# Optimization experiments

Hardware: AMD Instinct MI355X
Metric: run time of the kernel (lower is better)

Reference implementation:

```python
import jax, jax.numpy as jnp
import numpy as np

H = 19  # input_size == hidden_size

def setup_inputs() -> dict:
    key = jax.random.key(0)
    ks = jax.random.split(key, 7)
    seq_len, batch = 2048, 1024
    s = 1.0 / np.sqrt(H)  # PyTorch default uniform(-1/sqrt(H), 1/sqrt(H))
    x = jax.random.normal(ks[0], (seq_len, batch, H), dtype=jnp.float32)
    W_ih = jax.random.uniform(ks[1], (3 * H, H), jnp.float32, -s, s)
    W_hh = jax.random.uniform(ks[2], (3 * H, H), jnp.float32, -s, s)
    b_ih = jax.random.uniform(ks[3], (3 * H,), jnp.float32, -s, s)
    b_hh = jax.random.uniform(ks[4], (3 * H,), jnp.float32, -s, s)
    W_out = jax.random.uniform(ks[5], (1, H), jnp.float32, -s, s)
    b_out = jax.random.uniform(ks[6], (1,), jnp.float32, -s, s)
    return {"x": x, "W_ih": W_ih, "W_hh": W_hh, "b_ih": b_ih,
            "b_hh": b_hh, "W_out": W_out, "b_out": b_out}

def _gru(x, W_ih, W_hh, b_ih, b_hh):
    # Precompute all input projections in one big GEMM: [T, B, 3H]
    xg = jnp.einsum('tbi,gi->tbg', x, W_ih) + b_ih
    Whr, Whz, Whn = W_hh[:H], W_hh[H:2*H], W_hh[2*H:]
    bhr, bhz, bhn = b_hh[:H], b_hh[H:2*H], b_hh[2*H:]
    h0 = jnp.zeros(x.shape[1:2] + (H,), dtype=x.dtype)

    def step(h, xg_t):
        xr, xz, xn = xg_t[:, :H], xg_t[:, H:2*H], xg_t[:, 2*H:]
        r = jax.nn.sigmoid(xr + h @ Whr.T + bhr)
        z = jax.nn.sigmoid(xz + h @ Whz.T + bhz)
        n = jnp.tanh(xn + r * (h @ Whn.T + bhn))
        h_new = (1.0 - z) * n + z * h
        return h_new, h_new

    _, r_out = jax.lax.scan(step, h0, xg)  # r_out: [T, B, H]
    return r_out

def reference(x, W_ih, W_hh, b_ih, b_hh, W_out, b_out):
    r_out = _gru(x, W_ih, W_hh, b_ih, b_hh)
    return r_out @ W_out.T + b_out  # [T, B, 1]
```

## Files before the change

kernel.cpp:

```cpp
#include <hip/hip_runtime.h>
#include <math.h>

#define HH 19
#define NB 1024
#define TT 2048

typedef float v2f __attribute__((ext_vector_type(2)));
typedef unsigned u2 __attribute__((ext_vector_type(2)));

__device__ __forceinline__ float rl(float v, int l) {
  return __uint_as_float(__builtin_amdgcn_readlane(__float_as_uint(v), l));
}
__device__ __forceinline__ float frcp(float v) {
  return __builtin_amdgcn_rcpf(v);
}
__device__ __forceinline__ float fexp2(float v) {
#if __has_builtin(__builtin_amdgcn_exp2f)
  return __builtin_amdgcn_exp2f(v);
#else
  return exp2f(v);
#endif
}
__device__ __forceinline__ v2f vfma(v2f a, v2f b, v2f c) {
#if __has_builtin(__builtin_elementwise_fma)
  return __builtin_elementwise_fma(a, b, c);
#else
  v2f r; r.x = fmaf(a.x, b.x, c.x); r.y = fmaf(a.y, b.y, c.y); return r;
#endif
}

#if __has_builtin(__builtin_amdgcn_permlane32_swap)
#define HAVE_PLS 1
__device__ __forceinline__ u2 pls(float x) {
  unsigned u = __float_as_uint(x);
  return __builtin_amdgcn_permlane32_swap(u, u, false, false);
}
#else
#define HAVE_PLS 0
#endif

__global__ void __launch_bounds__(64)
__attribute__((amdgpu_waves_per_eu(1, 1)))
gru57_v2(const float* __restrict__ x, const float* __restrict__ Wih,
         const float* __restrict__ Whh, const float* __restrict__ bih,
         const float* __restrict__ bhh, const float* __restrict__ Wout,
         const float* __restrict__ bout, float* __restrict__ out)
{
  const int b = blockIdx.x;
  const int lane = threadIdx.x;

  const float L2E = 1.4426950408889634f;

  int row;
  if (lane < 32)      row = lane;
  else if (lane < 51) row = lane + 6;
  else if (lane < 57) row = lane - 19;
  else                row = 37;
  const bool isn = (row >= 2 * HH);
  const float scale = isn ? (2.0f * L2E) : L2E;

  v2f wx2[10], wh2[10], wo2[10];
#pragma unroll
  for (int j = 0; j < 10; ++j) {
    const int k0 = 2 * j, k1 = 2 * j + 1;
    wx2[j].x = Wih[row * HH + k0] * scale;
    wx2[j].y = (k1 < HH) ? Wih[row * HH + k1] * scale : 0.0f;
    wh2[j].x = Whh[row * HH + k0] * scale;
    wh2[j].y = (k1 < HH) ? Whh[row * HH + k1] * scale : 0.0f;
    wo2[j].x = Wout[k0];
    wo2[j].y = (k1 < HH) ? Wout[k1] : 0.0f;
  }
  const float bxv = bih[row] * scale, bhv = bhh[row] * scale;
  const float ax0 = isn ? bxv : (bxv + bhv);
  const float ah0 = isn ? bhv : 0.0f;
  const float bo  = bout[0];

  const int il = lane < HH ? lane : HH - 1;
  const int zaddr = ((il < 13) ? (19 + il) : (38 + il)) * 4;

#if HAVE_PLS
  bool loIsX;
  {
    unsigned l = (unsigned)lane;
    u2 pr = __builtin_amdgcn_permlane32_swap(l, l, false, false);
    loIsX = ((unsigned)__builtin_amdgcn_readlane((int)pr.x, 32) < 32u);
  }
#else
  const int loaddr = (lane & 31) * 4;
  const int hiaddr = ((lane & 31) | 32) * 4;
#endif

  float h = 0.0f;
  v2f sh2[10];
#pragma unroll
  for (int j = 0; j < 10; ++j) { sh2[j].x = 0.0f; sh2[j].y = 0.0f; }

  int vz;
  asm("v_mov_b32 %0, 0" : "=v"(vz));

  v2f xA[10], xB[10], xC[10], xD[10];
  xA[9].y = 0.0f; xB[9].y = 0.0f; xC[9].y = 0.0f; xD[9].y = 0.0f;

#define LOADROW(dst, trow) do {                                         \
    const float* _p = x + ((size_t)(trow) * NB + b) * HH + vz;          \
    _Pragma("unroll")                                                   \
    for (int _j = 0; _j < 9; ++_j) {                                    \
      dst[_j].x = _p[2 * _j];                                           \
      dst[_j].y = _p[2 * _j + 1];                                       \
    }                                                                   \
    dst[9].x = _p[18];                                                  \
  } while (0)

  LOADROW(xA, 0); LOADROW(xB, 1); LOADROW(xC, 2); LOADROW(xD, 3);

#if HAVE_PLS
#define LOBCAST(val, dst) do { u2 _s = pls(val);                        \
    dst = __uint_as_float(loIsX ? _s.x : _s.y); } while (0)
#define HIBCAST(val, dst) do { u2 _s = pls(val);                        \
    dst = __uint_as_float(loIsX ? _s.y : _s.x); } while (0)
#else
#define LOBCAST(val, dst) dst = __uint_as_float((unsigned)               \
    __builtin_amdgcn_ds_bpermute(loaddr, (int)__float_as_uint(val)))
#define HIBCAST(val, dst) dst = __uint_as_float((unsigned)               \
    __builtin_amdgcn_ds_bpermute(hiaddr, (int)__float_as_uint(val)))
#endif

#define STEP(xv, tcur) do {                                             \
    v2f axA = {ax0, 0.0f}, axB = {0.0f, 0.0f};                          \
    v2f ahA = {ah0, 0.0f}, ahB = {0.0f, 0.0f};                          \
    _Pragma("unroll")                                                   \
    for (int _j = 0; _j < 5; ++_j) {                                    \
      axA = vfma(xv[_j], wx2[_j], axA);                                 \
      ahA = vfma(sh2[_j], wh2[_j], ahA);                                \
    }                                                                   \
    _Pragma("unroll")                                                   \
    for (int _j = 5; _j < 10; ++_j) {                                   \
      axB = vfma(xv[_j], wx2[_j], axB);                                 \
      ahB = vfma(sh2[_j], wh2[_j], ahB);                                \
    }                                                                   \
    const v2f axv = axA + axB;                                          \
    const v2f ahv = ahA + ahB;                                          \
    const float prex = axv.x + axv.y;                                   \
    const float preh = ahv.x + ahv.y;                                   \
    const float pre  = prex + preh;                                     \
    const float sig  = frcp(1.0f + fexp2(-pre));                        \
                    \
    const int zzi = __builtin_amdgcn_ds_bpermute(                       \
        zaddr, (int)__float_as_uint(sig));                              \
                                  \
    float rr; LOBCAST(sig, rr);                                         \
    const float npre = fmaf(rr, preh, prex);                            \
    const float nn = fmaf(-2.0f, frcp(fexp2(npre) + 1.0f), 1.0f);       \
                                  \
    float nh; HIBCAST(nn, nh);                                          \
    const float zz = __uint_as_float((unsigned)zzi);                    \
    h = fmaf(zz, h - nh, nh);                                           \
    _Pragma("unroll")                                                   \
    for (int _j = 0; _j < 9; ++_j) {                                    \
      sh2[_j].x = rl(h, 2 * _j);                                        \
      sh2[_j].y = rl(h, 2 * _j + 1);                                    \
    }                                                                   \
    sh2[9].x = rl(h, 18); sh2[9].y = 0.0f;                              \
    v2f oA = {bo, 0.0f}, oB = {0.0f, 0.0f};                             \
    _Pragma("unroll")                                                   \
    for (int _j = 0; _j < 5; ++_j) oA = vfma(sh2[_j], wo2[_j], oA);     \
    _Pragma("unroll")                                                   \
    for (int _j = 5; _j < 10; ++_j) oB = vfma(sh2[_j], wo2[_j], oB);    \
    const v2f ov = oA + oB;                                             \
    if (lane == 0) out[(size_t)(tcur) * NB + b] = ov.x + ov.y;          \
  } while (0)

  for (int t = 0; t < TT; t += 4) {
    STEP(xA, t);
    { const int tn = (t + 4 < TT) ? t + 4 : TT - 1; LOADROW(xA, tn); }
    STEP(xB, t + 1);
    { const int tn = (t + 5 < TT) ? t + 5 : TT - 1; LOADROW(xB, tn); }
    STEP(xC, t + 2);
    { const int tn = (t + 6 < TT) ? t + 6 : TT - 1; LOADROW(xC, tn); }
    STEP(xD, t + 3);
    { const int tn = (t + 7 < TT) ? t + 7 : TT - 1; LOADROW(xD, tn); }
  }

#undef LOADROW
#undef STEP
#undef LOBCAST
#undef HIBCAST
}

extern "C" void kernel_launch(void* const* d_in, const int* in_sizes, int n_in,
                              void* d_out, int out_size, void* d_ws, size_t ws_size,
                              hipStream_t stream) {
  const float* x    = (const float*)d_in[0];
  const float* Wih  = (const float*)d_in[1];
  const float* Whh  = (const float*)d_in[2];
  const float* bih  = (const float*)d_in[3];
  const float* bhh  = (const float*)d_in[4];
  const float* Wout = (const float*)d_in[5];
  const float* bout = (const float*)d_in[6];
  float* out = (float*)d_out;

  gru57_v2<<<dim3(NB), dim3(64), 0, stream>>>(
      x, Wih, Whh, bih, bhh, Wout, bout, out);
}
```

Baseline: 624.0 us.

## Use fp16 dot2 for hidden/output projections and software-pipeline the input dot

Packs the broadcast hidden state into fp16 pairs so that the recurrent and output projections use v_dot2 instructions, and halves the number of readlane-produced values that are packed. It also computes the input projection for the next timestep off the critical path, interleaved with the current step, so the recurrence chain only holds the hidden-state dot and the activations. The risk is the precision loss from fp16 hidden state and weights accumulating over 2048 steps, and the removal of the HAVE_PLS=0 define may break the fallback path.

```diff
diff --git a/kernel.cpp b/kernel.cpp
--- a/kernel.cpp
+++ b/kernel.cpp
@@ -7,9 +7,10 @@
 
 typedef float v2f __attribute__((ext_vector_type(2)));
 typedef unsigned u2 __attribute__((ext_vector_type(2)));
-
-__device__ __forceinline__ float rl(float v, int l) {
-  return __uint_as_float(__builtin_amdgcn_readlane(__float_as_uint(v), l));
+typedef _Float16 v2h __attribute__((ext_vector_type(2)));
+
+__device__ __forceinline__ unsigned rlu(unsigned v, int l) {
+  return (unsigned)__builtin_amdgcn_readlane((int)v, l);
 }
 __device__ __forceinline__ float frcp(float v) {
   return __builtin_amdgcn_rcpf(v);
@@ -28,6 +29,20 @@
   v2f r; r.x = fmaf(a.x, b.x, c.x); r.y = fmaf(a.y, b.y, c.y); return r;
 #endif
 }
+
+#if __has_builtin(__builtin_amdgcn_fdot2)
+#define HAVE_DOT2 1
+__device__ __forceinline__ float dot2h(v2h w, unsigned packed, float acc) {
+  return __builtin_amdgcn_fdot2(w, __builtin_bit_cast(v2h, packed), acc, false);
+}
+#else
+#define HAVE_DOT2 0
+__device__ __forceinline__ float dot2h(v2h w, unsigned packed, float acc) {
+  const float fl = (float)__builtin_bit_cast(_Float16, (unsigned short)(packed & 0xffffu));
+  const float fh = (float)__builtin_bit_cast(_Float16, (unsigned short)(packed >> 16));
+  return fmaf((float)w.x, fl, fmaf((float)w.y, fh, acc));
+}
+#endif
 
 #if __has_builtin(__builtin_amdgcn_permlane32_swap)
 #define HAVE_PLS 1
@@ -35,13 +50,11 @@
   unsigned u = __float_as_uint(x);
   return __builtin_amdgcn_permlane32_swap(u, u, false, false);
 }
-#else
-#define HAVE_PLS 0
 #endif
 
 __global__ void __launch_bounds__(64)
 __attribute__((amdgpu_waves_per_eu(1, 1)))
-gru57_v2(const float* __restrict__ x, const float* __restrict__ Wih,
+gru57_v3(const float* __restrict__ x, const float* __restrict__ Wih,
          const float* __restrict__ Whh, const float* __restrict__ bih,
          const float* __restrict__ bhh, const float* __restrict__ Wout,
          const float* __restrict__ bout, float* __restrict__ out)
@@ -59,16 +72,17 @@
   const bool isn = (row >= 2 * HH);
   const float scale = isn ? (2.0f * L2E) : L2E;
 
-  v2f wx2[10], wh2[10], wo2[10];
+  v2f wx2[10];
+  v2h wh16[10], wo16[10];
 #pragma unroll
   for (int j = 0; j < 10; ++j) {
     const int k0 = 2 * j, k1 = 2 * j + 1;
     wx2[j].x = Wih[row * HH + k0] * scale;
     wx2[j].y = (k1 < HH) ? Wih[row * HH + k1] * scale : 0.0f;
-    wh2[j].x = Whh[row * HH + k0] * scale;
-    wh2[j].y = (k1 < HH) ? Whh[row * HH + k1] * scale : 0.0f;
-    wo2[j].x = Wout[k0];
-    wo2[j].y = (k1 < HH) ? Wout[k1] : 0.0f;
+    wh16[j].x = (_Float16)(Whh[row * HH + k0] * scale);
+    wh16[j].y = (_Float16)((k1 < HH) ? Whh[row * HH + k1] * scale : 0.0f);
+    wo16[j].x = (_Float16)Wout[k0];
+    wo16[j].y = (_Float16)((k1 < HH) ? Wout[k1] : 0.0f);
   }
   const float bxv = bih[row] * scale, bhv = bhh[row] * scale;
   const float ax0 = isn ? bxv : (bxv + bhv);
@@ -91,9 +105,9 @@
 #endif
 
   float h = 0.0f;
-  v2f sh2[10];
+  unsigned shp[10];
 #pragma unroll
-  for (int j = 0; j < 10; ++j) { sh2[j].x = 0.0f; sh2[j].y = 0.0f; }
+  for (int j = 0; j < 10; ++j) shp[j] = 0u;
 
   int vz;
   asm("v_mov_b32 %0, 0" : "=v"(vz));
@@ -111,7 +125,15 @@
     dst[9].x = _p[18];                                                  \
   } while (0)
 
-  LOADROW(xA, 0); LOADROW(xB, 1); LOADROW(xC, 2); LOADROW(xD, 3);
+#define XDOT(buf, dstvar) do {                                          \
+    v2f _aA = {ax0, 0.0f}, _aB = {0.0f, 0.0f};                          \
+    _Pragma("unroll")                                                   \
+    for (int _j = 0; _j < 5; ++_j)  _aA = vfma(buf[_j], wx2[_j], _aA);  \
+    _Pragma("unroll")                                                   \
+    for (int _j = 5; _j < 10; ++_j) _aB = vfma(buf[_j], wx2[_j], _aB);  \
+    const v2f _s = _aA + _aB;                                           \
+    dstvar = _s.x + _s.y;                                               \
+  } while (0)
 
 #if HAVE_PLS
 #define LOBCAST(val, dst) do { u2 _s = pls(val);                        \
@@ -119,70 +141,67 @@
 #define HIBCAST(val, dst) do { u2 _s = pls(val);                        \
     dst = __uint_as_float(loIsX ? _s.y : _s.x); } while (0)
 #else
-#define LOBCAST(val, dst) dst = __uint_as_float((unsigned)               \
+#define LOBCAST(val, dst) dst = __uint_as_float((unsigned)              \
     __builtin_amdgcn_ds_bpermute(loaddr, (int)__float_as_uint(val)))
-#define HIBCAST(val, dst) dst = __uint_as_float((unsigned)               \
+#define HIBCAST(val, dst) dst = __uint_as_float((unsigned)              \
     __builtin_amdgcn_ds_bpermute(hiaddr, (int)__float_as_uint(val)))
 #endif
 
-#define STEP(xv, tcur) do {                                             \
-    v2f axA = {ax0, 0.0f}, axB = {0.0f, 0.0f};                          \
-    v2f ahA = {ah0, 0.0f}, ahB = {0.0f, 0.0f};                          \
-    _Pragma("unroll")                                                   \
-    for (int _j = 0; _j < 5; ++_j) {                                    \
-      axA = vfma(xv[_j], wx2[_j], axA);                                 \
-      ahA = vfma(sh2[_j], wh2[_j], ahA);                                \
-    }                                                                   \
-    _Pragma("unroll")                                                   \
-    for (int _j = 5; _j < 10; ++_j) {                                   \
-      axB = vfma(xv[_j], wx2[_j], axB);                                 \
-      ahB = vfma(sh2[_j], wh2[_j], ahB);                                \
-    }                                                                   \
-    const v2f axv = axA + axB;                                          \
-    const v2f ahv = ahA + ahB;                                          \
-    const float prex = axv.x + axv.y;                                   \
-    const float preh = ahv.x + ahv.y;                                   \
+  LOADROW(xA, 0); LOADROW(xB, 1); LOADROW(xC, 2); LOADROW(xD, 3);
+  float prex;
+  XDOT(xA, prex);
+
+#define BODY(tcur, nbuf, lbuf) do {                                     \
+          \
+    float ahA = ah0, ahB = 0.0f;                                        \
+    _Pragma("unroll")                                                   \
+    for (int _j = 0; _j < 5; ++_j)  ahA = dot2h(wh16[_j], shp[_j], ahA);\
+    _Pragma("unroll")                                                   \
+    for (int _j = 5; _j < 10; ++_j) ahB = dot2h(wh16[_j], shp[_j], ahB);\
+              \
+    float prexN;                                                        \
+    XDOT(nbuf, prexN);                                                  \
+    { const int _tl = ((tcur) + 4 < TT) ? (tcur) + 4 : TT - 1;          \
+      LOADROW(lbuf, _tl); }                                             \
+                                                   \
+    const float preh = ahA + ahB;                                       \
     const float pre  = prex + preh;                                     \
     const float sig  = frcp(1.0f + fexp2(-pre));                        \
-                    \
     const int zzi = __builtin_amdgcn_ds_bpermute(                       \
         zaddr, (int)__float_as_uint(sig));                              \
-                                  \
     float rr; LOBCAST(sig, rr);                                         \
     const float npre = fmaf(rr, preh, prex);                            \
     const float nn = fmaf(-2.0f, frcp(fexp2(npre) + 1.0f), 1.0f);       \
-                                  \
     float nh; HIBCAST(nn, nh);                                          \
     const float zz = __uint_as_float((unsigned)zzi);                    \
     h = fmaf(zz, h - nh, nh);                                           \
-    _Pragma("unroll")                                                   \
-    for (int _j = 0; _j < 9; ++_j) {                                    \
-      sh2[_j].x = rl(h, 2 * _j);                                        \
-      sh2[_j].y = rl(h, 2 * _j + 1);                                    \
-    }                                                                   \
-    sh2[9].x = rl(h, 18); sh2[9].y = 0.0f;                              \
-    v2f oA = {bo, 0.0f}, oB = {0.0f, 0.0f};                             \
-    _Pragma("unroll")                                                   \
-    for (int _j = 0; _j < 5; ++_j) oA = vfma(sh2[_j], wo2[_j], oA);     \
-    _Pragma("unroll")                                                   \
-    for (int _j = 5; _j < 10; ++_j) oB = vfma(sh2[_j], wo2[_j], oB);    \
-    const v2f ov = oA + oB;                                             \
-    if (lane == 0) out[(size_t)(tcur) * NB + b] = ov.x + ov.y;          \
+           \
+    const unsigned hb = (unsigned)__builtin_bit_cast(                   \
+        unsigned short, (_Float16)h);                                   \
+    _Pragma("unroll")                                                   \
+    for (int _j = 0; _j < 9; ++_j)                                      \
+      shp[_j] = rlu(hb, 2 * _j) | (rlu(hb, 2 * _j + 1) << 16);          \
+    shp[9] = rlu(hb, 18);                                               \
+                                           \
+    float oA = bo, oB = 0.0f;                                           \
+    _Pragma("unroll")                                                   \
+    for (int _j = 0; _j < 5; ++_j)  oA = dot2h(wo16[_j], shp[_j], oA);  \
+    _Pragma("unroll")                                                   \
+    for (int _j = 5; _j < 10; ++_j) oB = dot2h(wo16[_j], shp[_j], oB);  \
+    if (lane == 0) out[(size_t)(tcur) * NB + b] = oA + oB;              \
+    prex = prexN;                                                       \
   } while (0)
 
   for (int t = 0; t < TT; t += 4) {
-    STEP(xA, t);
-    { const int tn = (t + 4 < TT) ? t + 4 : TT - 1; LOADROW(xA, tn); }
-    STEP(xB, t + 1);
-    { const int tn = (t + 5 < TT) ? t + 5 : TT - 1; LOADROW(xB, tn); }
-    STEP(xC, t + 2);
-    { const int tn = (t + 6 < TT) ? t + 6 : TT - 1; LOADROW(xC, tn); }
-    STEP(xD, t + 3);
-    { const int tn = (t + 7 < TT) ? t + 7 : TT - 1; LOADROW(xD, tn); }
+    BODY(t + 0, xB, xA);
+    BODY(t + 1, xC, xB);
+    BODY(t + 2, xD, xC);
+    BODY(t + 3, xA, xD);
   }
 
 #undef LOADROW
-#undef STEP
+#undef XDOT
+#undef BODY
 #undef LOBCAST
 #undef HIBCAST
 }
@@ -199,6 +218,6 @@
   const float* bout = (const float*)d_in[6];
   float* out = (float*)d_out;
 
-  gru57_v2<<<dim3(NB), dim3(64), 0, stream>>>(
+  gru57_v3<<<dim3(NB), dim3(64), 0, stream>>>(
       x, Wih, Whh, bih, bhh, Wout, bout, out);
 }
```

New measurement: 735.0 us. 17.8% more time.

## Load x per lane and compute next-step input projection ahead of recurrence

Applied to the files above, without the earlier changes.

Before, every lane loaded the full 19-element x row through uniform loads, held four such buffers (about 80 VGPRs), and did the input projection inline on the critical path. Now each lane loads a single x element, the row is broadcast with readlane, and the input projection for step t+1 is computed while step t's hidden-state dot product runs, so it sits off the serial dependency chain. This cuts vector memory instructions and register pressure. The cost is 19 extra readlane instructions per step.

```diff
diff --git a/kernel.cpp b/kernel.cpp
--- a/kernel.cpp
+++ b/kernel.cpp
@@ -8,7 +8,7 @@
 typedef float v2f __attribute__((ext_vector_type(2)));
 typedef unsigned u2 __attribute__((ext_vector_type(2)));
 
-__device__ __forceinline__ float rl(float v, int l) {
+__device__ __forceinline__ float rlf(float v, int l) {
   return __uint_as_float(__builtin_amdgcn_readlane(__float_as_uint(v), l));
 }
 __device__ __forceinline__ float frcp(float v) {
@@ -41,7 +41,7 @@
 
 __global__ void __launch_bounds__(64)
 __attribute__((amdgpu_waves_per_eu(1, 1)))
-gru57_v2(const float* __restrict__ x, const float* __restrict__ Wih,
+gru57_v4(const float* __restrict__ x, const float* __restrict__ Wih,
          const float* __restrict__ Whh, const float* __restrict__ bih,
          const float* __restrict__ bhh, const float* __restrict__ Wout,
          const float* __restrict__ bout, float* __restrict__ out)
@@ -95,23 +95,31 @@
 #pragma unroll
   for (int j = 0; j < 10; ++j) { sh2[j].x = 0.0f; sh2[j].y = 0.0f; }
 
-  int vz;
-  asm("v_mov_b32 %0, 0" : "=v"(vz));
-
-  v2f xA[10], xB[10], xC[10], xD[10];
-  xA[9].y = 0.0f; xB[9].y = 0.0f; xC[9].y = 0.0f; xD[9].y = 0.0f;
-
-#define LOADROW(dst, trow) do {                                         \
-    const float* _p = x + ((size_t)(trow) * NB + b) * HH + vz;          \
+  const int kx = lane < HH ? lane : HH - 1;
+  const float* __restrict__ xbase = x + (size_t)b * HH + kx;
+
+#define LOADX(dst, trow) do {                                           \
+    dst = xbase[(size_t)(trow) * (NB * HH)];                            \
+  } while (0)
+
+#define XBCAST(slot, xu) do {                                           \
     _Pragma("unroll")                                                   \
     for (int _j = 0; _j < 9; ++_j) {                                    \
-      dst[_j].x = _p[2 * _j];                                           \
-      dst[_j].y = _p[2 * _j + 1];                                       \
+      xu[_j].x = rlf(slot, 2 * _j);                                     \
+      xu[_j].y = rlf(slot, 2 * _j + 1);                                 \
     }                                                                   \
-    dst[9].x = _p[18];                                                  \
-  } while (0)
-
-  LOADROW(xA, 0); LOADROW(xB, 1); LOADROW(xC, 2); LOADROW(xD, 3);
+    xu[9].x = rlf(slot, 18); xu[9].y = 0.0f;                            \
+  } while (0)
+
+#define XDOT(xu, dstvar) do {                                           \
+    v2f _aA = {ax0, 0.0f}, _aB = {0.0f, 0.0f};                          \
+    _Pragma("unroll")                                                   \
+    for (int _j = 0; _j < 5; ++_j)  _aA = vfma(xu[_j], wx2[_j], _aA);   \
+    _Pragma("unroll")                                                   \
+    for (int _j = 5; _j < 10; ++_j) _aB = vfma(xu[_j], wx2[_j], _aB);   \
+    const v2f _s = _aA + _aB;                                           \
+    dstvar = _s.x + _s.y;                                               \
+  } while (0)
 
 #if HAVE_PLS
 #define LOBCAST(val, dst) do { u2 _s = pls(val);                        \
@@ -119,70 +127,78 @@
 #define HIBCAST(val, dst) do { u2 _s = pls(val);                        \
     dst = __uint_as_float(loIsX ? _s.y : _s.x); } while (0)
 #else
-#define LOBCAST(val, dst) dst = __uint_as_float((unsigned)               \
+#define LOBCAST(val, dst) dst = __uint_as_float((unsigned)              \
     __builtin_amdgcn_ds_bpermute(loaddr, (int)__float_as_uint(val)))
-#define HIBCAST(val, dst) dst = __uint_as_float((unsigned)               \
+#define HIBCAST(val, dst) dst = __uint_as_float((unsigned)              \
     __builtin_amdgcn_ds_bpermute(hiaddr, (int)__float_as_uint(val)))
 #endif
 
-#define STEP(xv, tcur) do {                                             \
-    v2f axA = {ax0, 0.0f}, axB = {0.0f, 0.0f};                          \
+  float xlA, xlB, xlC, xlD;
+  LOADX(xlA, 0); LOADX(xlB, 1); LOADX(xlC, 2); LOADX(xlD, 3);
+
+  float prex;
+  {
+    v2f xu0[10];
+    XBCAST(xlA, xu0);
+    XDOT(xu0, prex);
+  }
+
+#define BODY(tcur, nslot, lslot) do {                                   \
+                 \
     v2f ahA = {ah0, 0.0f}, ahB = {0.0f, 0.0f};                          \
     _Pragma("unroll")                                                   \
-    for (int _j = 0; _j < 5; ++_j) {                                    \
-      axA = vfma(xv[_j], wx2[_j], axA);                                 \
-      ahA = vfma(sh2[_j], wh2[_j], ahA);                                \
-    }                                                                   \
-    _Pragma("unroll")                                                   \
-    for (int _j = 5; _j < 10; ++_j) {                                   \
-      axB = vfma(xv[_j], wx2[_j], axB);                                 \
-      ahB = vfma(sh2[_j], wh2[_j], ahB);                                \
-    }                                                                   \
-    const v2f axv = axA + axB;                                          \
+    for (int _j = 0; _j < 5; ++_j)  ahA = vfma(sh2[_j], wh2[_j], ahA);  \
+    _Pragma("unroll")                                                   \
+    for (int _j = 5; _j < 10; ++_j) ahB = vfma(sh2[_j], wh2[_j], ahB);  \
+               \
+    float prexN;                                                        \
+    { v2f _xu[10];                                                      \
+      XBCAST(nslot, _xu);                                               \
+      XDOT(_xu, prexN); }                                               \
+    { const int _tl = ((tcur) + 4 < TT) ? (tcur) + 4 : TT - 1;          \
+      LOADX(lslot, _tl); }                                              \
+                                                   \
     const v2f ahv = ahA + ahB;                                          \
-    const float prex = axv.x + axv.y;                                   \
     const float preh = ahv.x + ahv.y;                                   \
     const float pre  = prex + preh;                                     \
     const float sig  = frcp(1.0f + fexp2(-pre));                        \
-                    \
     const int zzi = __builtin_amdgcn_ds_bpermute(                       \
         zaddr, (int)__float_as_uint(sig));                              \
-                                  \
     float rr; LOBCAST(sig, rr);                                         \
     const float npre = fmaf(rr, preh, prex);                            \
     const float nn = fmaf(-2.0f, frcp(fexp2(npre) + 1.0f), 1.0f);       \
-                                  \
     float nh; HIBCAST(nn, nh);                                          \
     const float zz = __uint_as_float((unsigned)zzi);                    \
     h = fmaf(zz, h - nh, nh);                                           \
+                  \
     _Pragma("unroll")                                                   \
     for (int _j = 0; _j < 9; ++_j) {                                    \
-      sh2[_j].x = rl(h, 2 * _j);                                        \
-      sh2[_j].y = rl(h, 2 * _j + 1);                                    \
+      sh2[_j].x = rlf(h, 2 * _j);                                       \
+      sh2[_j].y = rlf(h, 2 * _j + 1);                                   \
     }                                                                   \
-    sh2[9].x = rl(h, 18); sh2[9].y = 0.0f;                              \
+    sh2[9].x = rlf(h, 18); sh2[9].y = 0.0f;                             \
+        \
     v2f oA = {bo, 0.0f}, oB = {0.0f, 0.0f};                             \
     _Pragma("unroll")                                                   \
-    for (int _j = 0; _j < 5; ++_j) oA = vfma(sh2[_j], wo2[_j], oA);     \
+    for (int _j = 0; _j < 5; ++_j)  oA = vfma(sh2[_j], wo2[_j], oA);    \
     _Pragma("unroll")                                                   \
     for (int _j = 5; _j < 10; ++_j) oB = vfma(sh2[_j], wo2[_j], oB);    \
     const v2f ov = oA + oB;                                             \
     if (lane == 0) out[(size_t)(tcur) * NB + b] = ov.x + ov.y;          \
+    prex = prexN;                                                       \
   } while (0)
 
   for (int t = 0; t < TT; t += 4) {
-    STEP(xA, t);
-    { const int tn = (t + 4 < TT) ? t + 4 : TT - 1; LOADROW(xA, tn); }
-    STEP(xB, t + 1);
-    { const int tn = (t + 5 < TT) ? t + 5 : TT - 1; LOADROW(xB, tn); }
-    STEP(xC, t + 2);
-    { const int tn = (t + 6 < TT) ? t + 6 : TT - 1; LOADROW(xC, tn); }
-    STEP(xD, t + 3);
-    { const int tn = (t + 7 < TT) ? t + 7 : TT - 1; LOADROW(xD, tn); }
-  }
-
-#undef LOADROW
-#undef STEP
+    BODY(t + 0, xlB, xlA);
+    BODY(t + 1, xlC, xlB);
+    BODY(t + 2, xlD, xlC);
+    BODY(t + 3, xlA, xlD);
+  }
+
+#undef LOADX
+#undef XBCAST
+#undef XDOT
+#undef BODY
 #undef LOBCAST
 #undef HIBCAST
 }
@@ -199,6 +215,6 @@
   const float* bout = (const float*)d_in[6];
   float* out = (float*)d_out;
 
-  gru57_v2<<<dim3(NB), dim3(64), 0, stream>>>(
+  gru57_v4<<<dim3(NB), dim3(64), 0, stream>>>(
       x, Wih, Whh, bih, bhh, Wout, bout, out);
 }
```

New measurement: 555.2 us. 1.12x faster.
